# Performance work log

Measured on AMD Instinct MI355X. Metric: run time of the kernel, lower is better.

## Reference

```python
import jax, jax.numpy as jnp
import numpy as np

B, S, D_IN, D = 2, 192, 1024, 128  # batch, seq_len, input_dim, triaffine_dim


def setup_inputs() -> dict:
    key = jax.random.key(0)
    ks = jax.random.split(key, 10)
    g = lambda k, sh, sc: jax.random.normal(k, sh, jnp.float32) * sc
    return {
        "x": g(ks[0], (B, S, D_IN), 1.0),
        "Wp": g(ks[1], (D_IN, D), 0.02), "bp": jnp.zeros((D,), jnp.float32),
        "Wh": g(ks[2], (D_IN, D), 0.02), "bh": jnp.zeros((D,), jnp.float32),
        "Wt": g(ks[3], (D_IN, D), 0.02), "bt": jnp.zeros((D,), jnp.float32),
        "W_span_ph": g(ks[4], (D, D, D), 0.02),
        "W_span_pt": g(ks[5], (D, D, D), 0.02),
        "W_ph_sib": g(ks[6], (D, D, D), 0.02),
        "W_pt_sib": g(ks[7], (D, D, D), 0.02),
        "W_ph_cop": g(ks[8], (D, D, D), 0.02),
        "W_pt_cop": g(ks[9], (D, D, D), 0.02),
    }


def _mlp(x, W, b):
    # supar-style MLP: Linear + LeakyReLU(0.1); dropout is identity at eval time
    return jax.nn.leaky_relu(x @ W + b, negative_slope=0.1)


def _triaffine(x, y, z, w):
    # supar Triaffine (n_out=1, no bias): s[b,z,x,y] = x_i W_ikj z_k y_j
    wz = jnp.einsum('bzk,ikj->bzij', z, w)          # [b,s,d,d]
    return jnp.einsum('bxi,bzij,byj->bzxy', x, wz, y)  # [b,s,s,s]


def _sym(s):
    # s.triu() + s.triu(1).transpose(-1,-2) over last two dims
    n = s.shape[-1]
    up = jnp.triu(jnp.ones((n, n), bool))
    up1 = jnp.triu(jnp.ones((n, n), bool), 1)
    zero = jnp.zeros((), s.dtype)
    return jnp.where(up, s, zero) + jnp.swapaxes(jnp.where(up1, s, zero), -1, -2)


def reference(x, Wp, bp, Wh, bh, Wt, bt,
              W_span_ph, W_span_pt, W_ph_sib, W_pt_sib, W_ph_cop, W_pt_cop):
    p = _mlp(x, Wp, bp)
    sh = _mlp(x, Wh, bh)   # shared_span: sh_mlp = h_mlp
    st = _mlp(x, Wt, bt)   # shared_span: st_mlp = t_mlp
    span_pst = _sym(_triaffine(sh, st, p, W_span_pt))
    span_psh = _sym(_triaffine(sh, st, p, W_span_ph))
    ph_sib = _sym(_triaffine(sh, sh, p, W_ph_sib))
    pt_sib = _sym(_triaffine(st, st, p, W_pt_sib))
    # co-parent scores: [b,z,x,y] -> permute(0,2,3,1) -> [b,x,y,z]
    ph_cop = jnp.transpose(_triaffine(p, p, sh, W_ph_cop), (0, 2, 3, 1))
    pt_cop = jnp.transpose(_sym(_triaffine(p, p, st, W_pt_cop)), (0, 2, 3, 1))
    return (span_psh, span_pst, ph_sib, pt_sib, ph_cop, pt_cop)
```

## Files before the change

kernel.cpp:

```cpp
#include <hip/hip_runtime.h>

#define SS 192
#define DD 128
#define SAN 16384
#define PITCH 136

typedef short bf8v __attribute__((ext_vector_type(8)));
typedef float f4v  __attribute__((ext_vector_type(4)));

__device__ __forceinline__ unsigned short f2bf(float f) {
    union { float f; unsigned u; } v; v.f = f;
    unsigned r = v.u + 0x7fffu + ((v.u >> 16) & 1u);
    return (unsigned short)(r >> 16);
}

__device__ __forceinline__ f4v mfma16(bf8v a, bf8v b, f4v c) {
    return __builtin_amdgcn_mfma_f32_16x16x32_bf16(a, b, c, 0, 0, 0);
}

__global__ __launch_bounds__(256) void proj_kernel(
    const float* __restrict__ x,
    const float* __restrict__ Wp, const float* __restrict__ bp,
    const float* __restrict__ Wh, const float* __restrict__ bh,
    const float* __restrict__ Wt, const float* __restrict__ bt,
    unsigned short* __restrict__ Pb, unsigned short* __restrict__ SHb,
    unsigned short* __restrict__ STb)
{
    __shared__ float xs[8 * 1024];
    int r0 = blockIdx.x * 8;
    int w  = blockIdx.y;
    const float* W    = (w == 0) ? Wp : (w == 1) ? Wh : Wt;
    const float* bias = (w == 0) ? bp : (w == 1) ? bh : bt;
    unsigned short* O = (w == 0) ? Pb : (w == 1) ? SHb : STb;
    int tid = threadIdx.x;
    for (int u = tid; u < 2048; u += 256)
        *(float4*)(&xs[u * 4]) = *(const float4*)(&x[(size_t)r0 * 1024 + (size_t)u * 4]);
    __syncthreads();
    int col = tid & 127, rg = tid >> 7;
    float acc[4] = {0.f, 0.f, 0.f, 0.f};
    for (int k = 0; k < 1024; ++k) {
        float wv = W[(size_t)k * 128 + col];
        #pragma unroll
        for (int r = 0; r < 4; ++r) acc[r] += xs[(rg * 4 + r) * 1024 + k] * wv;
    }
    float bb = bias[col];
    #pragma unroll
    for (int r = 0; r < 4; ++r) {
        float v = acc[r] + bb;
        v = v > 0.f ? v : 0.1f * v;
        O[(size_t)(r0 + rg * 4 + r) * 128 + col] = f2bf(v);
    }
}

__global__ __launch_bounds__(256) void prep_rev(
    const float* __restrict__ w0, const float* __restrict__ w1,
    const float* __restrict__ w2, const float* __restrict__ w3,
    const float* __restrict__ w5, unsigned short* __restrict__ Wprep)
{
    __shared__ float tile[32][33];
    int sel = blockIdx.z;
    const float* in = (sel == 0) ? w0 : (sel == 1) ? w1 : (sel == 2) ? w2 : (sel == 3) ? w3 : w5;
    int slot = (sel == 4) ? 5 : sel;
    unsigned short* out = Wprep + (size_t)slot * 2097152;
    int i  = blockIdx.y;
    int kt = (blockIdx.x >> 2) * 32, jt = (blockIdx.x & 3) * 32;
    int tx = threadIdx.x & 31, ty = threadIdx.x >> 5;
    #pragma unroll
    for (int r = 0; r < 4; ++r) {
        int k = kt + ty + r * 8;
        tile[ty + r * 8][tx] = in[((size_t)i * 128 + k) * 128 + jt + tx];
    }
    __syncthreads();
    #pragma unroll
    for (int r = 0; r < 4; ++r) {
        int j = jt + ty + r * 8;
        out[((size_t)j * 128 + i) * 128 + kt + tx] = f2bf(tile[tx][ty + r * 8]);
    }
}

__global__ __launch_bounds__(256) void prep_cop(
    const float* __restrict__ in, unsigned short* __restrict__ Wprep)
{
    __shared__ float tile[32][33];
    unsigned short* out = Wprep + (size_t)4 * 2097152;
    int k  = blockIdx.y;
    int it = (blockIdx.x >> 2) * 32, jt = (blockIdx.x & 3) * 32;
    int tx = threadIdx.x & 31, ty = threadIdx.x >> 5;
    #pragma unroll
    for (int r = 0; r < 4; ++r) {
        int i = it + ty + r * 8;
        tile[ty + r * 8][tx] = in[((size_t)i * 128 + k) * 128 + jt + tx];
    }
    __syncthreads();
    #pragma unroll
    for (int r = 0; r < 4; ++r) {
        int j = jt + ty + r * 8;
        out[((size_t)j * 128 + k) * 128 + it + tx] = f2bf(tile[tx][ty + r * 8]);
    }
}

__global__ __launch_bounds__(256) void stageA(
    const unsigned short* __restrict__ Pb, const unsigned short* __restrict__ STb,
    const unsigned short* __restrict__ Wprep, unsigned short* __restrict__ SAout)
{
    __shared__ unsigned short BL[64 * PITCH];
    int slot = blockIdx.y;
    int n0 = blockIdx.x * 64;
    const unsigned short* A  = (slot == 5) ? STb : Pb;
    const unsigned short* Wn = Wprep + (size_t)slot * 2097152 + (size_t)n0 * 128;
    unsigned short* Oo = SAout + (size_t)slot * ((size_t)384 * SAN);
    int tid = threadIdx.x;
    for (int u = tid; u < 1024; u += 256) {
        int e = u * 8; int r = e >> 7; int c = e & 127;
        *(uint4*)(&BL[r * PITCH + c]) = *(const uint4*)(&Wn[e]);
    }
    __syncthreads();
    int wave = tid >> 6, lane = tid & 63, m = lane & 15, quad = lane >> 4;
    const unsigned short* br = &BL[(wave * 16 + m) * PITCH + quad * 8];
    bf8v b0 = *(const bf8v*)(br);
    bf8v b1 = *(const bf8v*)(br + 32);
    bf8v b2 = *(const bf8v*)(br + 64);
    bf8v b3 = *(const bf8v*)(br + 96);
    for (int mt = 0; mt < 24; ++mt) {
        const unsigned short* ar = A + (size_t)(mt * 16 + m) * 128 + quad * 8;
        f4v acc = {0.f, 0.f, 0.f, 0.f};
        acc = mfma16(*(const bf8v*)(ar),      b0, acc);
        acc = mfma16(*(const bf8v*)(ar + 32), b1, acc);
        acc = mfma16(*(const bf8v*)(ar + 64), b2, acc);
        acc = mfma16(*(const bf8v*)(ar + 96), b3, acc);
        unsigned short* orow = Oo + (size_t)(mt * 16) * SAN + n0 + wave * 16;
        #pragma unroll
        for (int r = 0; r < 4; ++r)
            orow[(size_t)(quad * 4 + r) * SAN + m] = f2bf(acc[r]);
    }
}

__global__ __launch_bounds__(256) void stageB_sym(
    const unsigned short* __restrict__ Pb, const unsigned short* __restrict__ SHb,
    const unsigned short* __restrict__ STb, const unsigned short* __restrict__ SA,
    float* __restrict__ out, float* __restrict__ tri_ws, int tbase)
{
    __shared__ unsigned short WZT[128 * PITCH];
    __shared__ unsigned short Tst[64 * PITCH];
    const size_t OUTN = (size_t)2 * SS * SS * SS;

    int t  = tbase + blockIdx.y;
    int bz = blockIdx.x;
    int b  = bz / SS;

    int slot; const unsigned short *X, *Y; float* O;
    if (t == 0)      { slot = 0; X = SHb; Y = STb; O = out + (size_t)bz * SS * SS; }
    else if (t == 1) { slot = 1; X = SHb; Y = STb; O = out + OUTN + (size_t)bz * SS * SS; }
    else if (t == 2) { slot = 2; X = SHb; Y = SHb; O = out + 2 * OUTN + (size_t)bz * SS * SS; }
    else if (t == 3) { slot = 3; X = STb; Y = STb; O = out + 3 * OUTN + (size_t)bz * SS * SS; }
    else             { slot = 5; X = Pb;  Y = Pb;  O = tri_ws + (size_t)bz * SS * SS; }

    const unsigned short* src = SA + ((size_t)slot * 384 + bz) * SAN;
    int tid = threadIdx.x;
    for (int u = tid; u < 2048; u += 256) {
        int e = u * 8; int j = e >> 7; int i = e & 127;
        *(uint4*)(&WZT[j * PITCH + i]) = *(const uint4*)(&src[e]);
    }
    __syncthreads();

    int wave = tid >> 6, lane = tid & 63, m = lane & 15, quad = lane >> 4;
    const int mt_tab[4][3] = {{0,7,9},{1,6,8},{2,5,10},{3,4,11}};

    const unsigned short* Xb = X + (size_t)b * SS * DD;
    const unsigned short* Yb = Y + (size_t)b * SS * DD;
    unsigned short* Trow = &Tst[wave * 16 * PITCH];
    const unsigned short* Ta = &Tst[(wave * 16 + m) * PITCH + quad * 8];

    for (int mi = 0; mi < 3; ++mi) {
        int mt = mt_tab[wave][mi];
        const unsigned short* xr = Xb + (size_t)(mt * 16 + m) * DD + quad * 8;
        bf8v a[4];
        a[0] = *(const bf8v*)(xr);
        a[1] = *(const bf8v*)(xr + 32);
        a[2] = *(const bf8v*)(xr + 64);
        a[3] = *(const bf8v*)(xr + 96);

        for (int nt = 0; nt < 8; nt += 2) {
            f4v acc0 = {0.f,0.f,0.f,0.f}, acc1 = {0.f,0.f,0.f,0.f};
            #pragma unroll
            for (int kk = 0; kk < 4; ++kk) {
                const unsigned short* bp0 = &WZT[(nt * 16 + m) * PITCH + kk * 32 + quad * 8];
                const unsigned short* bp1 = &WZT[((nt + 1) * 16 + m) * PITCH + kk * 32 + quad * 8];
                acc0 = mfma16(a[kk], *(const bf8v*)bp0, acc0);
                acc1 = mfma16(a[kk], *(const bf8v*)bp1, acc1);
            }
            #pragma unroll
            for (int r = 0; r < 4; ++r) {
                Trow[(quad * 4 + r) * PITCH + nt * 16 + m]       = f2bf(acc0[r]);
                Trow[(quad * 4 + r) * PITCH + (nt + 1) * 16 + m] = f2bf(acc1[r]);
            }
        }
        bf8v ta[4];
        ta[0] = *(const bf8v*)(Ta);
        ta[1] = *(const bf8v*)(Ta + 32);
        ta[2] = *(const bf8v*)(Ta + 64);
        ta[3] = *(const bf8v*)(Ta + 96);

        for (int yt = mt; yt < 12; ++yt) {
            f4v acc = {0.f,0.f,0.f,0.f};
            #pragma unroll
            for (int kk = 0; kk < 4; ++kk) {
                bf8v bv = *(const bf8v*)(Yb + (size_t)(yt * 16 + m) * DD + kk * 32 + quad * 8);
                acc = mfma16(ta[kk], bv, acc);
            }
            int xs_ = mt * 16, ys_ = yt * 16, cc = m;
            if (yt > mt) {
                #pragma unroll
                for (int r = 0; r < 4; ++r)
                    O[(size_t)(xs_ + quad * 4 + r) * SS + ys_ + cc] = acc[r];
                *(f4v*)(&O[(size_t)(ys_ + cc) * SS + xs_ + quad * 4]) = acc;
            } else {
                #pragma unroll
                for (int r = 0; r < 4; ++r) {
                    int rr = quad * 4 + r;
                    if (rr <= cc) O[(size_t)(xs_ + rr) * SS + ys_ + cc] = acc[r];
                    if (cc > rr)  O[(size_t)(ys_ + cc) * SS + xs_ + rr] = acc[r];
                }
            }
        }
    }
}

__global__ __launch_bounds__(256) void stageB_cop(
    const unsigned short* __restrict__ Pb, const unsigned short* __restrict__ SHb,
    const unsigned short* __restrict__ SA4, float* __restrict__ out4)
{
    __shared__ unsigned short MT[128 * PITCH];
    __shared__ unsigned short Tst[64 * PITCH];
    int bx = blockIdx.x;
    int b  = bx / SS;
    float* O = out4 + (size_t)bx * SS * SS;

    const unsigned short* src = SA4 + (size_t)bx * SAN;
    int tid = threadIdx.x;
    for (int u = tid; u < 2048; u += 256) {
        int e = u * 8; int j = e >> 7; int k = e & 127;
        *(uint4*)(&MT[j * PITCH + k]) = *(const uint4*)(&src[e]);
    }
    __syncthreads();

    int wave = tid >> 6, lane = tid & 63, m = lane & 15, quad = lane >> 4;
    unsigned short* Trow = &Tst[wave * 16 * PITCH];
    const unsigned short* Tb = &Tst[(wave * 16 + m) * PITCH + quad * 8];

    for (int zi = 0; zi < 3; ++zi) {
        int zt = wave * 3 + zi;
        const unsigned short* sr = SHb + (size_t)(b * SS + zt * 16 + m) * DD + quad * 8;
        bf8v a[4];
        a[0] = *(const bf8v*)(sr);
        a[1] = *(const bf8v*)(sr + 32);
        a[2] = *(const bf8v*)(sr + 64);
        a[3] = *(const bf8v*)(sr + 96);
        for (int jt = 0; jt < 8; jt += 2) {
            f4v acc0 = {0.f,0.f,0.f,0.f}, acc1 = {0.f,0.f,0.f,0.f};
            #pragma unroll
            for (int kk = 0; kk < 4; ++kk) {
                const unsigned short* bp0 = &MT[(jt * 16 + m) * PITCH + kk * 32 + quad * 8];
                const unsigned short* bp1 = &MT[((jt + 1) * 16 + m) * PITCH + kk * 32 + quad * 8];
                acc0 = mfma16(a[kk], *(const bf8v*)bp0, acc0);
                acc1 = mfma16(a[kk], *(const bf8v*)bp1, acc1);
            }
            #pragma unroll
            for (int r = 0; r < 4; ++r) {
                Trow[(quad * 4 + r) * PITCH + jt * 16 + m]       = f2bf(acc0[r]);
                Trow[(quad * 4 + r) * PITCH + (jt + 1) * 16 + m] = f2bf(acc1[r]);
            }
        }
        bf8v tb[4];
        tb[0] = *(const bf8v*)(Tb);
        tb[1] = *(const bf8v*)(Tb + 32);
        tb[2] = *(const bf8v*)(Tb + 64);
        tb[3] = *(const bf8v*)(Tb + 96);
        for (int yt = 0; yt < 12; ++yt) {
            f4v acc = {0.f,0.f,0.f,0.f};
            #pragma unroll
            for (int kk = 0; kk < 4; ++kk) {
                bf8v av = *(const bf8v*)(Pb + (size_t)(b * SS + yt * 16 + m) * DD + kk * 32 + quad * 8);
                acc = mfma16(av, tb[kk], acc);
            }
            #pragma unroll
            for (int r = 0; r < 4; ++r)
                O[(size_t)(yt * 16 + quad * 4 + r) * SS + zt * 16 + m] = acc[r];
        }
    }
}

__global__ __launch_bounds__(256) void transpose_cop(
    const float* __restrict__ tri, float* __restrict__ out5)
{
    __shared__ float tile[64][65];
    int b  = blockIdx.z;
    int z0 = blockIdx.y * 64;
    int q0 = blockIdx.x * 64;
    const float* src = tri + (size_t)b * SS * 36864;
    float* dst = out5 + (size_t)b * 36864 * SS;
    int tx = threadIdx.x & 63, ty = threadIdx.x >> 6;
    #pragma unroll
    for (int r = 0; r < 16; ++r) {
        int z = z0 + ty + r * 4;
        if (z < SS) tile[ty + r * 4][tx] = src[(size_t)z * 36864 + q0 + tx];
    }
    __syncthreads();
    #pragma unroll
    for (int r = 0; r < 16; ++r) {
        int q = q0 + ty + r * 4;
        if (z0 + tx < SS) dst[(size_t)q * SS + z0 + tx] = tile[tx][ty + r * 4];
    }
}

extern "C" void kernel_launch(void* const* d_in, const int* in_sizes, int n_in,
                              void* d_out, int out_size, void* d_ws, size_t ws_size,
                              hipStream_t stream)
{
    const float* x   = (const float*)d_in[0];
    const float* Wp  = (const float*)d_in[1];
    const float* bp  = (const float*)d_in[2];
    const float* Wh  = (const float*)d_in[3];
    const float* bh  = (const float*)d_in[4];
    const float* Wt  = (const float*)d_in[5];
    const float* bt  = (const float*)d_in[6];
    const float* W_span_ph = (const float*)d_in[7];
    const float* W_span_pt = (const float*)d_in[8];
    const float* W_ph_sib  = (const float*)d_in[9];
    const float* W_pt_sib  = (const float*)d_in[10];
    const float* W_ph_cop  = (const float*)d_in[11];
    const float* W_pt_cop  = (const float*)d_in[12];

    char* ws = (char*)d_ws;
    unsigned short* Pb    = (unsigned short*)ws;
    unsigned short* SHb   = Pb + 384 * 128;
    unsigned short* STb   = SHb + 384 * 128;
    unsigned short* Wprep = (unsigned short*)(ws + 294912);
    unsigned short* SA    = (unsigned short*)(ws + 294912 + (size_t)6 * 2097152 * 2);
    float* tri = (float*)SA;

    float* out  = (float*)d_out;
    const size_t OUTN = (size_t)2 * SS * SS * SS;

    proj_kernel<<<dim3(48, 3), 256, 0, stream>>>(x, Wp, bp, Wh, bh, Wt, bt, Pb, SHb, STb);
    prep_rev<<<dim3(16, 128, 5), 256, 0, stream>>>(W_span_ph, W_span_pt, W_ph_sib,
                                                   W_pt_sib, W_pt_cop, Wprep);
    prep_cop<<<dim3(16, 128), 256, 0, stream>>>(W_ph_cop, Wprep);
    stageA<<<dim3(256, 6), 256, 0, stream>>>(Pb, STb, Wprep, SA);
    stageB_sym<<<dim3(384, 4), 256, 0, stream>>>(Pb, SHb, STb, SA, out, tri, 0);
    stageB_cop<<<dim3(384), 256, 0, stream>>>(Pb, SHb, SA + (size_t)4 * 384 * SAN,
                                              out + 4 * OUTN);
    stageB_sym<<<dim3(384, 1), 256, 0, stream>>>(Pb, SHb, STb, SA, out, tri, 4);
    transpose_cop<<<dim3(576, 3, 2), 256, 0, stream>>>(tri, out + 5 * OUTN);
}
```

Before: 661.9 us.

## Fuse all triaffine stage-B variants into one kernel with direct cop output

The pt_cop path is reformulated so that W_pt_cop is prepared in the co-parent layout and contracted with P. Its results are written directly in the permuted [x,y,z] layout, with symmetric mirroring, instead of going through a float workspace and a separate transpose kernel. All six score tensors are now produced by a single stageB_all launch, and the sym path computes diagonal tiles separately and processes off-diagonal y tiles in pairs. This removes a full-size intermediate write, its read-back and two launches. In exchange the mirrored writes for pt_cop are strided scatters.

```diff
diff --git a/kernel.cpp b/kernel.cpp
--- a/kernel.cpp
+++ b/kernel.cpp
@@ -55,13 +55,12 @@
 __global__ __launch_bounds__(256) void prep_rev(
     const float* __restrict__ w0, const float* __restrict__ w1,
     const float* __restrict__ w2, const float* __restrict__ w3,
-    const float* __restrict__ w5, unsigned short* __restrict__ Wprep)
+    unsigned short* __restrict__ Wprep)
 {
     __shared__ float tile[32][33];
     int sel = blockIdx.z;
-    const float* in = (sel == 0) ? w0 : (sel == 1) ? w1 : (sel == 2) ? w2 : (sel == 3) ? w3 : w5;
-    int slot = (sel == 4) ? 5 : sel;
-    unsigned short* out = Wprep + (size_t)slot * 2097152;
+    const float* in = (sel == 0) ? w0 : (sel == 1) ? w1 : (sel == 2) ? w2 : w3;
+    unsigned short* out = Wprep + (size_t)sel * 2097152;
     int i  = blockIdx.y;
     int kt = (blockIdx.x >> 2) * 32, jt = (blockIdx.x & 3) * 32;
     int tx = threadIdx.x & 31, ty = threadIdx.x >> 5;
@@ -79,10 +78,13 @@
 }
 
 __global__ __launch_bounds__(256) void prep_cop(
-    const float* __restrict__ in, unsigned short* __restrict__ Wprep)
+    const float* __restrict__ in0, const float* __restrict__ in1,
+    unsigned short* __restrict__ Wprep)
 {
     __shared__ float tile[32][33];
-    unsigned short* out = Wprep + (size_t)4 * 2097152;
+    int sel = blockIdx.z;
+    const float* in = sel ? in1 : in0;
+    unsigned short* out = Wprep + (size_t)(4 + sel) * 2097152;
     int k  = blockIdx.y;
     int it = (blockIdx.x >> 2) * 32, jt = (blockIdx.x & 3) * 32;
     int tx = threadIdx.x & 31, ty = threadIdx.x >> 5;
@@ -100,13 +102,12 @@
 }
 
 __global__ __launch_bounds__(256) void stageA(
-    const unsigned short* __restrict__ Pb, const unsigned short* __restrict__ STb,
+    const unsigned short* __restrict__ Pb,
     const unsigned short* __restrict__ Wprep, unsigned short* __restrict__ SAout)
 {
     __shared__ unsigned short BL[64 * PITCH];
     int slot = blockIdx.y;
     int n0 = blockIdx.x * 64;
-    const unsigned short* A  = (slot == 5) ? STb : Pb;
     const unsigned short* Wn = Wprep + (size_t)slot * 2097152 + (size_t)n0 * 128;
     unsigned short* Oo = SAout + (size_t)slot * ((size_t)384 * SAN);
     int tid = threadIdx.x;
@@ -121,42 +122,43 @@
     bf8v b1 = *(const bf8v*)(br + 32);
     bf8v b2 = *(const bf8v*)(br + 64);
     bf8v b3 = *(const bf8v*)(br + 96);
-    for (int mt = 0; mt < 24; ++mt) {
-        const unsigned short* ar = A + (size_t)(mt * 16 + m) * 128 + quad * 8;
-        f4v acc = {0.f, 0.f, 0.f, 0.f};
-        acc = mfma16(*(const bf8v*)(ar),      b0, acc);
-        acc = mfma16(*(const bf8v*)(ar + 32), b1, acc);
-        acc = mfma16(*(const bf8v*)(ar + 64), b2, acc);
-        acc = mfma16(*(const bf8v*)(ar + 96), b3, acc);
-        unsigned short* orow = Oo + (size_t)(mt * 16) * SAN + n0 + wave * 16;
+    for (int mt = 0; mt < 24; mt += 2) {
+        const unsigned short* ar0 = Pb + (size_t)(mt * 16 + m) * 128 + quad * 8;
+        const unsigned short* ar1 = ar0 + 16 * 128;
+        f4v acc0 = {0.f, 0.f, 0.f, 0.f}, acc1 = {0.f, 0.f, 0.f, 0.f};
+        acc0 = mfma16(*(const bf8v*)(ar0),      b0, acc0);
+        acc1 = mfma16(*(const bf8v*)(ar1),      b0, acc1);
+        acc0 = mfma16(*(const bf8v*)(ar0 + 32), b1, acc0);
+        acc1 = mfma16(*(const bf8v*)(ar1 + 32), b1, acc1);
+        acc0 = mfma16(*(const bf8v*)(ar0 + 64), b2, acc0);
+        acc1 = mfma16(*(const bf8v*)(ar1 + 64), b2, acc1);
+        acc0 = mfma16(*(const bf8v*)(ar0 + 96), b3, acc0);
+        acc1 = mfma16(*(const bf8v*)(ar1 + 96), b3, acc1);
+        unsigned short* orow0 = Oo + (size_t)(mt * 16) * SAN + n0 + wave * 16;
+        unsigned short* orow1 = orow0 + (size_t)16 * SAN;
         #pragma unroll
-        for (int r = 0; r < 4; ++r)
-            orow[(size_t)(quad * 4 + r) * SAN + m] = f2bf(acc[r]);
-    }
-}
-
-__global__ __launch_bounds__(256) void stageB_sym(
+        for (int r = 0; r < 4; ++r) {
+            orow0[(size_t)(quad * 4 + r) * SAN + m] = f2bf(acc0[r]);
+            orow1[(size_t)(quad * 4 + r) * SAN + m] = f2bf(acc1[r]);
+        }
+    }
+}
+
+__global__ __launch_bounds__(256) void stageB_all(
     const unsigned short* __restrict__ Pb, const unsigned short* __restrict__ SHb,
     const unsigned short* __restrict__ STb, const unsigned short* __restrict__ SA,
-    float* __restrict__ out, float* __restrict__ tri_ws, int tbase)
+    float* __restrict__ out)
 {
     __shared__ unsigned short WZT[128 * PITCH];
     __shared__ unsigned short Tst[64 * PITCH];
     const size_t OUTN = (size_t)2 * SS * SS * SS;
 
-    int t  = tbase + blockIdx.y;
+    int t  = blockIdx.y;
     int bz = blockIdx.x;
     int b  = bz / SS;
-
-    int slot; const unsigned short *X, *Y; float* O;
-    if (t == 0)      { slot = 0; X = SHb; Y = STb; O = out + (size_t)bz * SS * SS; }
-    else if (t == 1) { slot = 1; X = SHb; Y = STb; O = out + OUTN + (size_t)bz * SS * SS; }
-    else if (t == 2) { slot = 2; X = SHb; Y = SHb; O = out + 2 * OUTN + (size_t)bz * SS * SS; }
-    else if (t == 3) { slot = 3; X = STb; Y = STb; O = out + 3 * OUTN + (size_t)bz * SS * SS; }
-    else             { slot = 5; X = Pb;  Y = Pb;  O = tri_ws + (size_t)bz * SS * SS; }
-
-    const unsigned short* src = SA + ((size_t)slot * 384 + bz) * SAN;
     int tid = threadIdx.x;
+
+    const unsigned short* src = SA + ((size_t)t * 384 + bz) * SAN;
     for (int u = tid; u < 2048; u += 256) {
         int e = u * 8; int j = e >> 7; int i = e & 127;
         *(uint4*)(&WZT[j * PITCH + i]) = *(const uint4*)(&src[e]);
@@ -164,152 +166,201 @@
     __syncthreads();
 
     int wave = tid >> 6, lane = tid & 63, m = lane & 15, quad = lane >> 4;
-    const int mt_tab[4][3] = {{0,7,9},{1,6,8},{2,5,10},{3,4,11}};
-
-    const unsigned short* Xb = X + (size_t)b * SS * DD;
-    const unsigned short* Yb = Y + (size_t)b * SS * DD;
     unsigned short* Trow = &Tst[wave * 16 * PITCH];
     const unsigned short* Ta = &Tst[(wave * 16 + m) * PITCH + quad * 8];
 
-    for (int mi = 0; mi < 3; ++mi) {
-        int mt = mt_tab[wave][mi];
-        const unsigned short* xr = Xb + (size_t)(mt * 16 + m) * DD + quad * 8;
-        bf8v a[4];
-        a[0] = *(const bf8v*)(xr);
-        a[1] = *(const bf8v*)(xr + 32);
-        a[2] = *(const bf8v*)(xr + 64);
-        a[3] = *(const bf8v*)(xr + 96);
-
-        for (int nt = 0; nt < 8; nt += 2) {
-            f4v acc0 = {0.f,0.f,0.f,0.f}, acc1 = {0.f,0.f,0.f,0.f};
-            #pragma unroll
-            for (int kk = 0; kk < 4; ++kk) {
-                const unsigned short* bp0 = &WZT[(nt * 16 + m) * PITCH + kk * 32 + quad * 8];
-                const unsigned short* bp1 = &WZT[((nt + 1) * 16 + m) * PITCH + kk * 32 + quad * 8];
-                acc0 = mfma16(a[kk], *(const bf8v*)bp0, acc0);
-                acc1 = mfma16(a[kk], *(const bf8v*)bp1, acc1);
+    if (t < 4) {
+        const unsigned short* X = (t == 3) ? STb : SHb;
+        const unsigned short* Y = (t == 2) ? SHb : STb;
+        float* O = out + (size_t)t * OUTN + (size_t)bz * SS * SS;
+
+        const int mt_tab[4][3] = {{0,7,9},{1,6,8},{2,5,10},{3,4,11}};
+        const unsigned short* Xb = X + (size_t)b * SS * DD;
+        const unsigned short* Yb = Y + (size_t)b * SS * DD;
+
+        for (int mi = 0; mi < 3; ++mi) {
+            int mt = mt_tab[wave][mi];
+            const unsigned short* xr = Xb + (size_t)(mt * 16 + m) * DD + quad * 8;
+            bf8v a[4];
+            a[0] = *(const bf8v*)(xr);
+            a[1] = *(const bf8v*)(xr + 32);
+            a[2] = *(const bf8v*)(xr + 64);
+            a[3] = *(const bf8v*)(xr + 96);
+
+            for (int nt = 0; nt < 8; nt += 2) {
+                f4v acc0 = {0.f,0.f,0.f,0.f}, acc1 = {0.f,0.f,0.f,0.f};
+                #pragma unroll
+                for (int kk = 0; kk < 4; ++kk) {
+                    const unsigned short* bp0 = &WZT[(nt * 16 + m) * PITCH + kk * 32 + quad * 8];
+                    const unsigned short* bp1 = &WZT[((nt + 1) * 16 + m) * PITCH + kk * 32 + quad * 8];
+                    acc0 = mfma16(a[kk], *(const bf8v*)bp0, acc0);
+                    acc1 = mfma16(a[kk], *(const bf8v*)bp1, acc1);
+                }
+                #pragma unroll
+                for (int r = 0; r < 4; ++r) {
+                    Trow[(quad * 4 + r) * PITCH + nt * 16 + m]       = f2bf(acc0[r]);
+                    Trow[(quad * 4 + r) * PITCH + (nt + 1) * 16 + m] = f2bf(acc1[r]);
+                }
             }
-            #pragma unroll
-            for (int r = 0; r < 4; ++r) {
-                Trow[(quad * 4 + r) * PITCH + nt * 16 + m]       = f2bf(acc0[r]);
-                Trow[(quad * 4 + r) * PITCH + (nt + 1) * 16 + m] = f2bf(acc1[r]);
+            bf8v ta[4];
+            ta[0] = *(const bf8v*)(Ta);
+            ta[1] = *(const bf8v*)(Ta + 32);
+            ta[2] = *(const bf8v*)(Ta + 64);
+            ta[3] = *(const bf8v*)(Ta + 96);
+
+            int xs_ = mt * 16, cc = m;
+            {
+                f4v acc = {0.f,0.f,0.f,0.f};
+                #pragma unroll
+                for (int kk = 0; kk < 4; ++kk) {
+                    bf8v bv = *(const bf8v*)(Yb + (size_t)(mt * 16 + m) * DD + kk * 32 + quad * 8);
+                    acc = mfma16(ta[kk], bv, acc);
+                }
+                #pragma unroll
+                for (int r = 0; r < 4; ++r) {
+                    int rr = quad * 4 + r;
+                    if (rr <= cc) O[(size_t)(xs_ + rr) * SS + xs_ + cc] = acc[r];
+                    if (cc > rr)  O[(size_t)(xs_ + cc) * SS + xs_ + rr] = acc[r];
+                }
+            }
+            for (int yt = mt + 1; yt < 12; yt += 2) {
+                bool pair = (yt + 1 < 12);
+                const unsigned short* yb0 = Yb + (size_t)(yt * 16 + m) * DD + quad * 8;
+                f4v acc0 = {0.f,0.f,0.f,0.f}, acc1 = {0.f,0.f,0.f,0.f};
+                if (pair) {
+                    const unsigned short* yb1 = yb0 + 16 * DD;
+                    #pragma unroll
+                    for (int kk = 0; kk < 4; ++kk) {
+                        bf8v bv0 = *(const bf8v*)(yb0 + kk * 32);
+                        bf8v bv1 = *(const bf8v*)(yb1 + kk * 32);
+                        acc0 = mfma16(ta[kk], bv0, acc0);
+                        acc1 = mfma16(ta[kk], bv1, acc1);
+                    }
+                } else {
+                    #pragma unroll
+                    for (int kk = 0; kk < 4; ++kk)
+                        acc0 = mfma16(ta[kk], *(const bf8v*)(yb0 + kk * 32), acc0);
+                }
+                int ys0 = yt * 16;
+                #pragma unroll
+                for (int r = 0; r < 4; ++r)
+                    O[(size_t)(xs_ + quad * 4 + r) * SS + ys0 + cc] = acc0[r];
+                *(f4v*)(&O[(size_t)(ys0 + cc) * SS + xs_ + quad * 4]) = acc0;
+                if (pair) {
+                    int ys1 = ys0 + 16;
+                    #pragma unroll
+                    for (int r = 0; r < 4; ++r)
+                        O[(size_t)(xs_ + quad * 4 + r) * SS + ys1 + cc] = acc1[r];
+                    *(f4v*)(&O[(size_t)(ys1 + cc) * SS + xs_ + quad * 4]) = acc1;
+                }
             }
         }
-        bf8v ta[4];
-        ta[0] = *(const bf8v*)(Ta);
-        ta[1] = *(const bf8v*)(Ta + 32);
-        ta[2] = *(const bf8v*)(Ta + 64);
-        ta[3] = *(const bf8v*)(Ta + 96);
-
-        for (int yt = mt; yt < 12; ++yt) {
-            f4v acc = {0.f,0.f,0.f,0.f};
-            #pragma unroll
-            for (int kk = 0; kk < 4; ++kk) {
-                bf8v bv = *(const bf8v*)(Yb + (size_t)(yt * 16 + m) * DD + kk * 32 + quad * 8);
-                acc = mfma16(ta[kk], bv, acc);
+    } else {
+        const unsigned short* Zsrc = (t == 4) ? SHb : STb;
+        int x  = bz - b * SS;
+        int xt = x >> 4;
+        float* Od = out + (size_t)t * OUTN + (size_t)bz * SS * SS;
+        float* Om = out + (size_t)t * OUTN + (size_t)b * SS * SS * SS;
+
+        for (int zi = 0; zi < 3; ++zi) {
+            int zt = wave * 3 + zi;
+            const unsigned short* sr = Zsrc + (size_t)(b * SS + zt * 16 + m) * DD + quad * 8;
+            bf8v a[4];
+            a[0] = *(const bf8v*)(sr);
+            a[1] = *(const bf8v*)(sr + 32);
+            a[2] = *(const bf8v*)(sr + 64);
+            a[3] = *(const bf8v*)(sr + 96);
+            for (int jt = 0; jt < 8; jt += 2) {
+                f4v acc0 = {0.f,0.f,0.f,0.f}, acc1 = {0.f,0.f,0.f,0.f};
+                #pragma unroll
+                for (int kk = 0; kk < 4; ++kk) {
+                    const unsigned short* bp0 = &WZT[(jt * 16 + m) * PITCH + kk * 32 + quad * 8];
+                    const unsigned short* bp1 = &WZT[((jt + 1) * 16 + m) * PITCH + kk * 32 + quad * 8];
+                    acc0 = mfma16(a[kk], *(const bf8v*)bp0, acc0);
+                    acc1 = mfma16(a[kk], *(const bf8v*)bp1, acc1);
+                }
+                #pragma unroll
+                for (int r = 0; r < 4; ++r) {
+                    Trow[(quad * 4 + r) * PITCH + jt * 16 + m]       = f2bf(acc0[r]);
+                    Trow[(quad * 4 + r) * PITCH + (jt + 1) * 16 + m] = f2bf(acc1[r]);
+                }
             }
-            int xs_ = mt * 16, ys_ = yt * 16, cc = m;
-            if (yt > mt) {
-                #pragma unroll
-                for (int r = 0; r < 4; ++r)
-                    O[(size_t)(xs_ + quad * 4 + r) * SS + ys_ + cc] = acc[r];
-                *(f4v*)(&O[(size_t)(ys_ + cc) * SS + xs_ + quad * 4]) = acc;
+            bf8v tb[4];
+            tb[0] = *(const bf8v*)(Ta);
+            tb[1] = *(const bf8v*)(Ta + 32);
+            tb[2] = *(const bf8v*)(Ta + 64);
+            tb[3] = *(const bf8v*)(Ta + 96);
+
+            const unsigned short* Pbase = Pb + (size_t)b * SS * DD;
+            int zc = zt * 16 + m;
+
+            if (t == 4) {
+                for (int yt = 0; yt < 12; yt += 2) {
+                    const unsigned short* p0 = Pbase + (size_t)(yt * 16 + m) * DD + quad * 8;
+                    const unsigned short* p1 = p0 + 16 * DD;
+                    f4v acc0 = {0.f,0.f,0.f,0.f}, acc1 = {0.f,0.f,0.f,0.f};
+                    #pragma unroll
+                    for (int kk = 0; kk < 4; ++kk) {
+                        bf8v av0 = *(const bf8v*)(p0 + kk * 32);
+                        bf8v av1 = *(const bf8v*)(p1 + kk * 32);
+                        acc0 = mfma16(av0, tb[kk], acc0);
+                        acc1 = mfma16(av1, tb[kk], acc1);
+                    }
+                    #pragma unroll
+                    for (int r = 0; r < 4; ++r) {
+                        Od[(size_t)(yt * 16 + quad * 4 + r) * SS + zc]       = acc0[r];
+                        Od[(size_t)((yt + 1) * 16 + quad * 4 + r) * SS + zc] = acc1[r];
+                    }
+                }
             } else {
-                #pragma unroll
-                for (int r = 0; r < 4; ++r) {
-                    int rr = quad * 4 + r;
-                    if (rr <= cc) O[(size_t)(xs_ + rr) * SS + ys_ + cc] = acc[r];
-                    if (cc > rr)  O[(size_t)(ys_ + cc) * SS + xs_ + rr] = acc[r];
+                {
+                    const unsigned short* p0 = Pbase + (size_t)(xt * 16 + m) * DD + quad * 8;
+                    f4v acc = {0.f,0.f,0.f,0.f};
+                    #pragma unroll
+                    for (int kk = 0; kk < 4; ++kk)
+                        acc = mfma16(*(const bf8v*)(p0 + kk * 32), tb[kk], acc);
+                    #pragma unroll
+                    for (int r = 0; r < 4; ++r) {
+                        int y = xt * 16 + quad * 4 + r;
+                        if (y >= x) Od[(size_t)y * SS + zc] = acc[r];
+                        if (y > x)  Om[(size_t)y * SS * SS + (size_t)x * SS + zc] = acc[r];
+                    }
+                }
+                for (int yt = xt + 1; yt < 12; yt += 2) {
+                    bool pair = (yt + 1 < 12);
+                    const unsigned short* p0 = Pbase + (size_t)(yt * 16 + m) * DD + quad * 8;
+                    f4v acc0 = {0.f,0.f,0.f,0.f}, acc1 = {0.f,0.f,0.f,0.f};
+                    if (pair) {
+                        const unsigned short* p1 = p0 + 16 * DD;
+                        #pragma unroll
+                        for (int kk = 0; kk < 4; ++kk) {
+                            bf8v av0 = *(const bf8v*)(p0 + kk * 32);
+                            bf8v av1 = *(const bf8v*)(p1 + kk * 32);
+                            acc0 = mfma16(av0, tb[kk], acc0);
+                            acc1 = mfma16(av1, tb[kk], acc1);
+                        }
+                    } else {
+                        #pragma unroll
+                        for (int kk = 0; kk < 4; ++kk)
+                            acc0 = mfma16(*(const bf8v*)(p0 + kk * 32), tb[kk], acc0);
+                    }
+                    #pragma unroll
+                    for (int r = 0; r < 4; ++r) {
+                        int y0 = yt * 16 + quad * 4 + r;
+                        Od[(size_t)y0 * SS + zc] = acc0[r];
+                        Om[(size_t)y0 * SS * SS + (size_t)x * SS + zc] = acc0[r];
+                    }
+                    if (pair) {
+                        #pragma unroll
+                        for (int r = 0; r < 4; ++r) {
+                            int y1 = (yt + 1) * 16 + quad * 4 + r;
+                            Od[(size_t)y1 * SS + zc] = acc1[r];
+                            Om[(size_t)y1 * SS * SS + (size_t)x * SS + zc] = acc1[r];
+                        }
+                    }
                 }
             }
         }
-    }
-}
-
-__global__ __launch_bounds__(256) void stageB_cop(
-    const unsigned short* __restrict__ Pb, const unsigned short* __restrict__ SHb,
-    const unsigned short* __restrict__ SA4, float* __restrict__ out4)
-{
-    __shared__ unsigned short MT[128 * PITCH];
-    __shared__ unsigned short Tst[64 * PITCH];
-    int bx = blockIdx.x;
-    int b  = bx / SS;
-    float* O = out4 + (size_t)bx * SS * SS;
-
-    const unsigned short* src = SA4 + (size_t)bx * SAN;
-    int tid = threadIdx.x;
-    for (int u = tid; u < 2048; u += 256) {
-        int e = u * 8; int j = e >> 7; int k = e & 127;
-        *(uint4*)(&MT[j * PITCH + k]) = *(const uint4*)(&src[e]);
-    }
-    __syncthreads();
-
-    int wave = tid >> 6, lane = tid & 63, m = lane & 15, quad = lane >> 4;
-    unsigned short* Trow = &Tst[wave * 16 * PITCH];
-    const unsigned short* Tb = &Tst[(wave * 16 + m) * PITCH + quad * 8];
-
-    for (int zi = 0; zi < 3; ++zi) {
-        int zt = wave * 3 + zi;
-        const unsigned short* sr = SHb + (size_t)(b * SS + zt * 16 + m) * DD + quad * 8;
-        bf8v a[4];
-        a[0] = *(const bf8v*)(sr);
-        a[1] = *(const bf8v*)(sr + 32);
-        a[2] = *(const bf8v*)(sr + 64);
-        a[3] = *(const bf8v*)(sr + 96);
-        for (int jt = 0; jt < 8; jt += 2) {
-            f4v acc0 = {0.f,0.f,0.f,0.f}, acc1 = {0.f,0.f,0.f,0.f};
-            #pragma unroll
-            for (int kk = 0; kk < 4; ++kk) {
-                const unsigned short* bp0 = &MT[(jt * 16 + m) * PITCH + kk * 32 + quad * 8];
-                const unsigned short* bp1 = &MT[((jt + 1) * 16 + m) * PITCH + kk * 32 + quad * 8];
-                acc0 = mfma16(a[kk], *(const bf8v*)bp0, acc0);
-                acc1 = mfma16(a[kk], *(const bf8v*)bp1, acc1);
-            }
-            #pragma unroll
-            for (int r = 0; r < 4; ++r) {
-                Trow[(quad * 4 + r) * PITCH + jt * 16 + m]       = f2bf(acc0[r]);
-                Trow[(quad * 4 + r) * PITCH + (jt + 1) * 16 + m] = f2bf(acc1[r]);
-            }
-        }
-        bf8v tb[4];
-        tb[0] = *(const bf8v*)(Tb);
-        tb[1] = *(const bf8v*)(Tb + 32);
-        tb[2] = *(const bf8v*)(Tb + 64);
-        tb[3] = *(const bf8v*)(Tb + 96);
-        for (int yt = 0; yt < 12; ++yt) {
-            f4v acc = {0.f,0.f,0.f,0.f};
-            #pragma unroll
-            for (int kk = 0; kk < 4; ++kk) {
-                bf8v av = *(const bf8v*)(Pb + (size_t)(b * SS + yt * 16 + m) * DD + kk * 32 + quad * 8);
-                acc = mfma16(av, tb[kk], acc);
-            }
-            #pragma unroll
-            for (int r = 0; r < 4; ++r)
-                O[(size_t)(yt * 16 + quad * 4 + r) * SS + zt * 16 + m] = acc[r];
-        }
-    }
-}
-
-__global__ __launch_bounds__(256) void transpose_cop(
-    const float* __restrict__ tri, float* __restrict__ out5)
-{
-    __shared__ float tile[64][65];
-    int b  = blockIdx.z;
-    int z0 = blockIdx.y * 64;
-    int q0 = blockIdx.x * 64;
-    const float* src = tri + (size_t)b * SS * 36864;
-    float* dst = out5 + (size_t)b * 36864 * SS;
-    int tx = threadIdx.x & 63, ty = threadIdx.x >> 6;
-    #pragma unroll
-    for (int r = 0; r < 16; ++r) {
-        int z = z0 + ty + r * 4;
-        if (z < SS) tile[ty + r * 4][tx] = src[(size_t)z * 36864 + q0 + tx];
-    }
-    __syncthreads();
-    #pragma unroll
-    for (int r = 0; r < 16; ++r) {
-        int q = q0 + ty + r * 4;
-        if (z0 + tx < SS) dst[(size_t)q * SS + z0 + tx] = tile[tx][ty + r * 4];
     }
 }
 
@@ -337,19 +388,13 @@
     unsigned short* STb   = SHb + 384 * 128;
     unsigned short* Wprep = (unsigned short*)(ws + 294912);
     unsigned short* SA    = (unsigned short*)(ws + 294912 + (size_t)6 * 2097152 * 2);
-    float* tri = (float*)SA;
 
     float* out  = (float*)d_out;
-    const size_t OUTN = (size_t)2 * SS * SS * SS;
 
     proj_kernel<<<dim3(48, 3), 256, 0, stream>>>(x, Wp, bp, Wh, bh, Wt, bt, Pb, SHb, STb);
-    prep_rev<<<dim3(16, 128, 5), 256, 0, stream>>>(W_span_ph, W_span_pt, W_ph_sib,
-                                                   W_pt_sib, W_pt_cop, Wprep);
-    prep_cop<<<dim3(16, 128), 256, 0, stream>>>(W_ph_cop, Wprep);
-    stageA<<<dim3(256, 6), 256, 0, stream>>>(Pb, STb, Wprep, SA);
-    stageB_sym<<<dim3(384, 4), 256, 0, stream>>>(Pb, SHb, STb, SA, out, tri, 0);
-    stageB_cop<<<dim3(384), 256, 0, stream>>>(Pb, SHb, SA + (size_t)4 * 384 * SAN,
-                                              out + 4 * OUTN);
-    stageB_sym<<<dim3(384, 1), 256, 0, stream>>>(Pb, SHb, STb, SA, out, tri, 4);
-    transpose_cop<<<dim3(576, 3, 2), 256, 0, stream>>>(tri, out + 5 * OUTN);
-}
+    prep_rev<<<dim3(16, 128, 4), 256, 0, stream>>>(W_span_ph, W_span_pt, W_ph_sib,
+                                                   W_pt_sib, Wprep);
+    prep_cop<<<dim3(16, 128, 2), 256, 0, stream>>>(W_ph_cop, W_pt_cop, Wprep);
+    stageA<<<dim3(256, 6), 256, 0, stream>>>(Pb, Wprep, SA);
+    stageB_all<<<dim3(384, 6), 256, 0, stream>>>(Pb, SHb, STb, SA, out);
+}
```

Result: faster. 640.9 us (-3.2%).
